# Performance work log

Measured on AMD Instinct MI355X. Metric: run time of the kernel, lower is better.

## Reference

```python
import jax, jax.numpy as jnp
import numpy as np
from jax import lax

K = 3      # reassembly kernel size
UP = 2     # upsample factor


def setup_inputs() -> dict:
    key = jax.random.key(0)
    ks = jax.random.split(key, 4)
    N, C, H, W = 4, 256, 128, 128
    outC = 256
    x = jax.random.normal(ks[0], (N, C, H, W), dtype=jnp.float32)
    w_down = jax.random.normal(ks[1], (C // 4, C), dtype=jnp.float32) * 0.05
    b_down = jnp.zeros((C // 4,), dtype=jnp.float32)
    w_enc = jax.random.normal(ks[2], (UP * UP * K * K, C // 4, K, K), dtype=jnp.float32) * 0.05
    b_enc = jnp.zeros((UP * UP * K * K,), dtype=jnp.float32)
    w_out = jax.random.normal(ks[3], (outC, C), dtype=jnp.float32) * 0.05
    b_out = jnp.zeros((outC,), dtype=jnp.float32)
    return {"x": x, "w_down": w_down, "b_down": b_down,
            "w_enc": w_enc, "b_enc": b_enc, "w_out": w_out, "b_out": b_out}


def _carafe_upsample(x, w_down, b_down, w_enc, b_enc, w_out, b_out):
    N, C, H, W = x.shape
    k2, up2 = K * K, UP * UP
    # kernel prediction branch: 1x1 down conv, 3x3 encoder conv
    t = jnp.einsum('oc,nchw->nohw', w_down, x) + b_down[None, :, None, None]
    enc = lax.conv_general_dilated(
        t, w_enc, window_strides=(1, 1), padding=((K // 2, K // 2), (K // 2, K // 2)),
        dimension_numbers=('NCHW', 'OIHW', 'NCHW')) + b_enc[None, :, None, None]
    # torch encoder channel layout is kk*up2 + ij; pixel_shuffle + softmax(dim=1)
    # + unfold(up,up) is equivalent to softmax over the k^2 axis here.
    enc = enc.reshape(N, k2, up2, H, W)
    kernel = jax.nn.softmax(enc, axis=1)                 # [N,k2,up2,H,W]
    kernel = kernel.transpose(0, 3, 4, 1, 2)             # [N,H,W,k2,up2]
    # extract kxk patches (zero pad), ordering di*K+dj matches torch unfold
    pad = K // 2
    xp = jnp.pad(x, ((0, 0), (0, 0), (pad, pad), (pad, pad)))
    patches = jnp.stack([xp[:, :, di:di + H, dj:dj + W]
                         for di in range(K) for dj in range(K)], axis=-1)  # [N,C,H,W,k2]
    # per-pixel reassembly matmul
    out = jnp.einsum('nchwk,nhwkq->nchwq', patches, kernel)  # [N,C,H,W,up2]
    # pixel_shuffle: channel index c*up2 + i*UP + j -> (h*UP+i, w*UP+j)
    out = out.reshape(N, C, H, W, UP, UP).transpose(0, 1, 2, 4, 3, 5)
    out = out.reshape(N, C, H * UP, W * UP)
    # final 1x1 conv
    return jnp.einsum('oc,nchw->nohw', w_out, out) + b_out[None, :, None, None]


def reference(x, w_down, b_down, w_enc, b_enc, w_out, b_out):
    return _carafe_upsample(x, w_down, b_down, w_enc, b_enc, w_out, b_out)
```

## Files before the change

### kernel.cpp

```cpp
#include <hip/hip_runtime.h>
#include <hip/hip_bf16.h>
#include <stddef.h>

typedef __attribute__((ext_vector_type(8))) short short8;
typedef __attribute__((ext_vector_type(4))) short short4v;
typedef __attribute__((ext_vector_type(4))) unsigned short ushort4v;
typedef __attribute__((ext_vector_type(4))) float floatx4;

#define N_ 4
#define C_ 256
#define H_ 128
#define W_ 128
#define HW_ (H_*W_)
#define NPX_ (N_*HW_)
#define E_ 36
#define OC_ 256

static __device__ __forceinline__ unsigned short f2bf(float f) {
    union { float f; unsigned u; } v; v.f = f;
    unsigned r = v.u + 0x7fff + ((v.u >> 16) & 1);
    return (unsigned short)(r >> 16);
}
static __device__ __forceinline__ float bf2f(unsigned short s) {
    union { unsigned u; float f; } v; v.u = ((unsigned)s) << 16;
    return v.f;
}

__global__ __launch_bounds__(256) void k_prep(const float* __restrict__ wo,
                                              const float* __restrict__ wd,
                                              short* __restrict__ wcomb,
                                              const float* __restrict__ we,
                                              unsigned short* __restrict__ wBT) {
    int bx = blockIdx.x;
    if (bx < 80) {
        int i = (bx * 256 + threadIdx.x) * 4;
        int row = i >> 8, c = i & 255;
        const float* src = (row < 256) ? &wo[row * 256 + c] : &wd[(row - 256) * 256 + c];
        float4 v = *(const float4*)src;
        short4v s;
        s.x = (short)f2bf(v.x); s.y = (short)f2bf(v.y);
        s.z = (short)f2bf(v.z); s.w = (short)f2bf(v.w);
        *(short4v*)&wcomb[i] = s;
    } else {
        int idx = (bx - 80) * 256 + threadIdx.x;
        if (idx < 48 * 576) {
            int e = idx / 576;
            int k = idx - e * 576;
            int tap = k >> 6, c = k & 63;
            float v = (e < E_) ? we[((size_t)e * 64 + c) * 9 + tap] : 0.f;
            wBT[idx] = f2bf(v);
        }
    }
}

__global__ __launch_bounds__(512, 3) void k_gemm(
    const float* __restrict__ x, const short* __restrict__ wcomb,
    const float* __restrict__ bd,
    unsigned short* __restrict__ Gq, unsigned short* __restrict__ t)
{
    __shared__ short Asm[2][320 * 40];
    __shared__ short Bsm[2][128 * 40];

    int tid = threadIdx.x;
    int bx = blockIdx.x;
    int n = bx >> 7;
    int px0 = (bx & 127) * 128;

    int lane = tid & 63;
    int wave = tid >> 6;
    int wm = wave >> 2, wn = wave & 3;

    int ao = tid >> 1, ah = tid & 1;
    int bpx = tid & 127, bcq = tid >> 7;
    bool hasExtra = (tid < 128);

    const float* xb = x + (size_t)n * C_ * HW_ + px0 + bpx;
    const short* wr  = wcomb + ao * C_ + ah * 16;
    const short* wr2 = wcomb + (256 + (tid >> 1)) * C_ + (tid & 1) * 16;

    short8 a0, a1, a2, a3;
    float xg[8];

    auto issue = [&](int c0) {
        a0 = *(const short8*)(wr + c0);
        a1 = *(const short8*)(wr + c0 + 8);
        if (hasExtra) {
            a2 = *(const short8*)(wr2 + c0);
            a3 = *(const short8*)(wr2 + c0 + 8);
        }
        #pragma unroll
        for (int j = 0; j < 8; j++)
            xg[j] = xb[(size_t)(c0 + bcq * 8 + j) * HW_];
    };
    auto commit = [&](int buf) {
        short* ad = &Asm[buf][ao * 40 + ah * 16];
        *(short8*)ad = a0;
        *(short8*)(ad + 8) = a1;
        if (hasExtra) {
            short* ad2 = &Asm[buf][(256 + (tid >> 1)) * 40 + (tid & 1) * 16];
            *(short8*)ad2 = a2;
            *(short8*)(ad2 + 8) = a3;
        }
        short8 bv;
        #pragma unroll
        for (int j = 0; j < 8; j++) bv[j] = (short)f2bf(xg[j]);
        *(short8*)&Bsm[buf][bpx * 40 + bcq * 8] = bv;
    };

    floatx4 acc[10][2];
    #pragma unroll
    for (int fm = 0; fm < 10; fm++) {
        acc[fm][0] = (floatx4)0.f;
        acc[fm][1] = (floatx4)0.f;
    }

    issue(0);
    commit(0);
    __syncthreads();

    for (int kc = 0; kc < 8; kc++) {
        int cur = kc & 1;
        if (kc < 7) issue((kc + 1) * 32);
        short8 bfrag[2];
        #pragma unroll
        for (int fn = 0; fn < 2; fn++) {
            int col = wn * 32 + fn * 16 + (lane & 15);
            bfrag[fn] = *(const short8*)&Bsm[cur][col * 40 + (lane >> 4) * 8];
        }
        #pragma unroll
        for (int fm = 0; fm < 10; fm++) {
            int rbase = (fm < 8) ? (wm * 128 + fm * 16) : (256 + wm * 32 + (fm - 8) * 16);
            int row = rbase + (lane & 15);
            short8 af = *(const short8*)&Asm[cur][row * 40 + (lane >> 4) * 8];
            acc[fm][0] = __builtin_amdgcn_mfma_f32_16x16x32_bf16(af, bfrag[0], acc[fm][0], 0, 0, 0);
            acc[fm][1] = __builtin_amdgcn_mfma_f32_16x16x32_bf16(af, bfrag[1], acc[fm][1], 0, 0, 0);
        }
        if (kc < 7) {
            commit(cur ^ 1);
            __syncthreads();
        }
    }
    #pragma unroll
    for (int fm = 0; fm < 8; fm++) {
        int oq = wm * 32 + fm * 4 + (lane >> 4);
        #pragma unroll
        for (int fn = 0; fn < 2; fn++) {
            int col = px0 + wn * 32 + fn * 16 + (lane & 15);
            ushort4v v;
            v.x = f2bf(acc[fm][fn][0]);
            v.y = f2bf(acc[fm][fn][1]);
            v.z = f2bf(acc[fm][fn][2]);
            v.w = f2bf(acc[fm][fn][3]);
            *(ushort4v*)&Gq[(((size_t)n * 64 + oq) * HW_ + col) * 4] = v;
        }
    }
    #pragma unroll
    for (int f8 = 0; f8 < 2; f8++) {
        int ot = wm * 32 + f8 * 16 + ((lane >> 4) << 2);
        float b0 = bd[ot + 0], b1 = bd[ot + 1], b2 = bd[ot + 2], b3 = bd[ot + 3];
        #pragma unroll
        for (int fn = 0; fn < 2; fn++) {
            int col = px0 + wn * 32 + fn * 16 + (lane & 15);
            ushort4v r;
            r.x = f2bf(acc[8 + f8][fn][0] + b0);
            r.y = f2bf(acc[8 + f8][fn][1] + b1);
            r.z = f2bf(acc[8 + f8][fn][2] + b2);
            r.w = f2bf(acc[8 + f8][fn][3] + b3);
            *(ushort4v*)&t[((size_t)n * HW_ + col) * 64 + ot] = r;
        }
    }
}

__global__ __launch_bounds__(256) void k_enc(
    const unsigned short* __restrict__ t, const unsigned short* __restrict__ wBT,
    const float* __restrict__ be, float* __restrict__ kern)
{
    __shared__ unsigned short Tl[198 * 64];
    __shared__ float El[64 * 48];

    int bx = blockIdx.x;
    int n = bx >> 8, h = (bx >> 1) & 127, wh = bx & 1;
    int w0 = wh * 64;
    int tid = threadIdx.x;

    for (int idx = tid; idx < 1584; idx += 256) {
        int r = idx >> 3, ch = idx & 7;
        int di = r / 66, rr = r - di * 66;
        int hh = h + di - 1, ww = w0 + rr - 1;
        short8 v = {0,0,0,0,0,0,0,0};
        if (hh >= 0 && hh < H_ && ww >= 0 && ww < W_)
            v = *(const short8*)&t[((size_t)(n * H_ + hh) * W_ + ww) * 64 + ch * 8];
        int us = (r * 64 + ch * 8) ^ ((r & 7) << 3);
        *(short8*)&Tl[us] = v;
    }
    __syncthreads();

    int lane = tid & 63, wave = tid >> 6;
    int m0 = wave * 16;

    floatx4 acc[3];
    acc[0] = (floatx4)0.f; acc[1] = (floatx4)0.f; acc[2] = (floatx4)0.f;

    int pxl = m0 + (lane & 15);
    int kq = (lane >> 4) * 8;
    #pragma unroll
    for (int kc = 0; kc < 18; kc++) {
        const int tap = kc >> 1, chalf = kc & 1;
        const int di = tap / 3, dj = tap % 3;
        int r = di * 66 + pxl + dj;
        int us = (r * 64 + chalf * 32 + kq) ^ ((r & 7) << 3);
        short8 af = *(const short8*)&Tl[us];
        #pragma unroll
        for (int fn = 0; fn < 3; fn++) {
            int nn = fn * 16 + (lane & 15);
            short8 bf = *(const short8*)&wBT[(size_t)nn * 576 + kc * 32 + kq];
            acc[fn] = __builtin_amdgcn_mfma_f32_16x16x32_bf16(af, bf, acc[fn], 0, 0, 0);
        }
    }
    #pragma unroll
    for (int fn = 0; fn < 3; fn++)
        #pragma unroll
        for (int i = 0; i < 4; i++) {
            int px = m0 + (lane >> 4) * 4 + i;
            El[px * 48 + fn * 16 + (lane & 15)] = acc[fn][i];
        }
    __syncthreads();

    int sp = tid >> 2, q = tid & 3;
    float l[9];
    #pragma unroll
    for (int k = 0; k < 9; k++) l[k] = El[sp * 48 + k * 4 + q] + be[k * 4 + q];
    float m = l[0];
    #pragma unroll
    for (int k = 1; k < 9; k++) m = fmaxf(m, l[k]);
    float ex[9], s = 0.f;
    #pragma unroll
    for (int k = 0; k < 9; k++) { ex[k] = __expf(l[k] - m); s += ex[k]; }
    float inv = 1.f / s;
    int pxg = n * HW_ + h * W_ + w0 + sp;
    #pragma unroll
    for (int k = 0; k < 9; k++)
        kern[(size_t)(k * 4 + q) * NPX_ + pxg] = ex[k] * inv;
}

__global__ __launch_bounds__(256) void k_up(
    const unsigned short* __restrict__ Gq, const float* __restrict__ kern,
    const float* __restrict__ bo, float* __restrict__ y)
{
    int bx = blockIdx.x;
    int x7 = bx & 7;
    int g  = bx >> 3;
    int hbhi = g & 7;
    int og = (g >> 3) & 7;
    int n  = g >> 6;
    int hb = hbhi * 8 + x7;

    int tid = threadIdx.x;
    int h = hb * 2 + (tid >> 7);
    int w = tid & 127;
    int idxp = n * HW_ + h * W_ + w;

    float kv[36];
    #pragma unroll
    for (int e = 0; e < E_; e++)
        kv[e] = kern[(size_t)e * NPX_ + idxp];

    int off[9]; bool val[9];
    #pragma unroll
    for (int di = 0; di < 3; di++) {
        int hh = h + di - 1;
        bool hvv = (hh >= 0 && hh < H_);
        int hc = hvv ? hh : h;
        #pragma unroll
        for (int dj = 0; dj < 3; dj++) {
            int ww = w + dj - 1;
            bool wvv = (ww >= 0 && ww < W_);
            int wc = wvv ? ww : w;
            off[di * 3 + dj] = hc * W_ + wc;
            val[di * 3 + dj] = hvv && wvv;
        }
    }

    const unsigned short* Gb = Gq + ((size_t)n * 64 + og * 8) * HW_ * 4;
    size_t ybase = ((size_t)n * OC_ + og * 32) * (4 * HW_) + (size_t)(2 * h) * 256 + 2 * w;

    #pragma unroll 2
    for (int j = 0; j < 8; j++) {
        const unsigned short* Gj = Gb + (size_t)j * HW_ * 4;
        float b0 = bo[og * 32 + j * 4 + 0];
        float b1 = bo[og * 32 + j * 4 + 1];
        float b2 = bo[og * 32 + j * 4 + 2];
        float b3 = bo[og * 32 + j * 4 + 3];
        float a[4][4];
        #pragma unroll
        for (int s = 0; s < 4; s++) { a[0][s] = b0; a[1][s] = b1; a[2][s] = b2; a[3][s] = b3; }
        #pragma unroll
        for (int k = 0; k < 9; k++) {
            ushort4v gv = *(const ushort4v*)(Gj + (size_t)off[k] * 4);
            float g0 = val[k] ? bf2f(gv.x) : 0.f;
            float g1 = val[k] ? bf2f(gv.y) : 0.f;
            float g2 = val[k] ? bf2f(gv.z) : 0.f;
            float g3 = val[k] ? bf2f(gv.w) : 0.f;
            #pragma unroll
            for (int s = 0; s < 4; s++) {
                float kw = kv[k * 4 + s];
                a[0][s] = fmaf(g0, kw, a[0][s]);
                a[1][s] = fmaf(g1, kw, a[1][s]);
                a[2][s] = fmaf(g2, kw, a[2][s]);
                a[3][s] = fmaf(g3, kw, a[3][s]);
            }
        }
        #pragma unroll
        for (int i = 0; i < 4; i++) {
            float* yp = y + ybase + (size_t)(j * 4 + i) * (4 * HW_);
            float2 r0; r0.x = a[i][0]; r0.y = a[i][1];
            float2 r1; r1.x = a[i][2]; r1.y = a[i][3];
            *(float2*)yp = r0;
            *(float2*)(yp + 256) = r1;
        }
    }
}

extern "C" void kernel_launch(void* const* d_in, const int* in_sizes, int n_in,
                              void* d_out, int out_size, void* d_ws, size_t ws_size,
                              hipStream_t stream) {
    const float* x  = (const float*)d_in[0];
    const float* wd = (const float*)d_in[1];
    const float* bd = (const float*)d_in[2];
    const float* we = (const float*)d_in[3];
    const float* be = (const float*)d_in[4];
    const float* wo = (const float*)d_in[5];
    const float* bo = (const float*)d_in[6];
    float* y = (float*)d_out;

    unsigned short* t = (unsigned short*)d_ws;
    float* kern = (float*)(t + (size_t)NPX_ * 64);
    short* wcomb = (short*)(kern + (size_t)E_ * NPX_);
    unsigned short* wBT = (unsigned short*)(wcomb + (size_t)320 * C_);
    unsigned short* Gq  = wBT + (size_t)48 * 576;

    k_prep<<<188,  256, 0, stream>>>(wo, wd, wcomb, we, wBT);
    k_gemm<<<512,  512, 0, stream>>>(x, wcomb, bd, Gq, t);
    k_enc <<<1024, 256, 0, stream>>>(t, wBT, be, kern);
    k_up  <<<2048, 256, 0, stream>>>(Gq, kern, bo, y);
}
```

Before: 148.8 us.

## Widen enc conv tile to full row and prefetch weights into registers

The encoder 3x3 conv kernel now processes a full 128-pixel row per block instead of half a row. Each wave computes two M fragments, which shrinks halo reloads from the 3-row neighbourhood and halves the block count. B-operand weight fragments are prefetched into a 3-slot register ring two k-steps ahead rather than loaded from global memory right before each MFMA. The LDS tile is reused for the softmax staging buffer with a padded stride of 49. The trade-off is more registers and LDS per block and fewer blocks, which may lower occupancy.

```diff
diff --git a/kernel.cpp b/kernel.cpp
--- a/kernel.cpp
+++ b/kernel.cpp
@@ -175,18 +175,26 @@
     const unsigned short* __restrict__ t, const unsigned short* __restrict__ wBT,
     const float* __restrict__ be, float* __restrict__ kern)
 {
-    __shared__ unsigned short Tl[198 * 64];
-    __shared__ float El[64 * 48];
+    __shared__ short Tl[390 * 64];
+    float* El = (float*)Tl;
 
     int bx = blockIdx.x;
-    int n = bx >> 8, h = (bx >> 1) & 127, wh = bx & 1;
-    int w0 = wh * 64;
+    int n = bx >> 7, h = bx & 127;
     int tid = threadIdx.x;
-
-    for (int idx = tid; idx < 1584; idx += 256) {
+    int lane = tid & 63, wave = tid >> 6;
+
+    short8 bpre[3][3];
+    const unsigned short* wB0 = wBT + (size_t)(lane & 15) * 576 + (lane >> 4) * 8;
+    #pragma unroll
+    for (int p = 0; p < 2; p++)
+        #pragma unroll
+        for (int fn = 0; fn < 3; fn++)
+            bpre[p][fn] = *(const short8*)(wB0 + fn * 16 * 576 + p * 32);
+
+    for (int idx = tid; idx < 3120; idx += 256) {
         int r = idx >> 3, ch = idx & 7;
-        int di = r / 66, rr = r - di * 66;
-        int hh = h + di - 1, ww = w0 + rr - 1;
+        int di = r / 130, rr = r - di * 130;
+        int hh = h + di - 1, ww = rr - 1;
         short8 v = {0,0,0,0,0,0,0,0};
         if (hh >= 0 && hh < H_ && ww >= 0 && ww < W_)
             v = *(const short8*)&t[((size_t)(n * H_ + hh) * W_ + ww) * 64 + ch * 8];
@@ -195,52 +203,69 @@
     }
     __syncthreads();
 
-    int lane = tid & 63, wave = tid >> 6;
-    int m0 = wave * 16;
-
-    floatx4 acc[3];
-    acc[0] = (floatx4)0.f; acc[1] = (floatx4)0.f; acc[2] = (floatx4)0.f;
-
-    int pxl = m0 + (lane & 15);
+    floatx4 acc[2][3];
+    #pragma unroll
+    for (int mf = 0; mf < 2; mf++)
+        #pragma unroll
+        for (int fn = 0; fn < 3; fn++)
+            acc[mf][fn] = (floatx4)0.f;
+
+    int pxw = wave * 32 + (lane & 15);
     int kq = (lane >> 4) * 8;
+
     #pragma unroll
     for (int kc = 0; kc < 18; kc++) {
+        if (kc < 16) {
+            int slot = (kc + 2) % 3;
+            #pragma unroll
+            for (int fn = 0; fn < 3; fn++)
+                bpre[slot][fn] = *(const short8*)(wB0 + fn * 16 * 576 + (kc + 2) * 32);
+        }
+        const int cur = kc % 3;
         const int tap = kc >> 1, chalf = kc & 1;
         const int di = tap / 3, dj = tap % 3;
-        int r = di * 66 + pxl + dj;
-        int us = (r * 64 + chalf * 32 + kq) ^ ((r & 7) << 3);
-        short8 af = *(const short8*)&Tl[us];
-        #pragma unroll
-        for (int fn = 0; fn < 3; fn++) {
-            int nn = fn * 16 + (lane & 15);
-            short8 bf = *(const short8*)&wBT[(size_t)nn * 576 + kc * 32 + kq];
-            acc[fn] = __builtin_amdgcn_mfma_f32_16x16x32_bf16(af, bf, acc[fn], 0, 0, 0);
-        }
-    }
-    #pragma unroll
-    for (int fn = 0; fn < 3; fn++)
-        #pragma unroll
-        for (int i = 0; i < 4; i++) {
-            int px = m0 + (lane >> 4) * 4 + i;
-            El[px * 48 + fn * 16 + (lane & 15)] = acc[fn][i];
-        }
+        #pragma unroll
+        for (int mf = 0; mf < 2; mf++) {
+            int r = di * 130 + pxw + mf * 16 + dj;
+            int us = (r * 64 + chalf * 32 + kq) ^ ((r & 7) << 3);
+            short8 af = *(const short8*)&Tl[us];
+            #pragma unroll
+            for (int fn = 0; fn < 3; fn++)
+                acc[mf][fn] = __builtin_amdgcn_mfma_f32_16x16x32_bf16(af, bpre[cur][fn], acc[mf][fn], 0, 0, 0);
+        }
+    }
     __syncthreads();
 
-    int sp = tid >> 2, q = tid & 3;
-    float l[9];
-    #pragma unroll
-    for (int k = 0; k < 9; k++) l[k] = El[sp * 48 + k * 4 + q] + be[k * 4 + q];
-    float m = l[0];
-    #pragma unroll
-    for (int k = 1; k < 9; k++) m = fmaxf(m, l[k]);
-    float ex[9], s = 0.f;
-    #pragma unroll
-    for (int k = 0; k < 9; k++) { ex[k] = __expf(l[k] - m); s += ex[k]; }
-    float inv = 1.f / s;
-    int pxg = n * HW_ + h * W_ + w0 + sp;
-    #pragma unroll
-    for (int k = 0; k < 9; k++)
-        kern[(size_t)(k * 4 + q) * NPX_ + pxg] = ex[k] * inv;
+    #pragma unroll
+    for (int mf = 0; mf < 2; mf++)
+        #pragma unroll
+        for (int fn = 0; fn < 3; fn++)
+            #pragma unroll
+            for (int i = 0; i < 4; i++) {
+                int px = wave * 32 + mf * 16 + (lane >> 4) * 4 + i;
+                El[px * 49 + fn * 16 + (lane & 15)] = acc[mf][fn][i];
+            }
+    __syncthreads();
+
+    int sp = tid >> 1;
+    int pxg = n * HW_ + h * W_ + sp;
+    #pragma unroll
+    for (int qq = 0; qq < 2; qq++) {
+        int q = (tid & 1) * 2 + qq;
+        float l[9];
+        #pragma unroll
+        for (int k = 0; k < 9; k++) l[k] = El[sp * 49 + k * 4 + q] + be[k * 4 + q];
+        float m = l[0];
+        #pragma unroll
+        for (int k = 1; k < 9; k++) m = fmaxf(m, l[k]);
+        float ex[9], s = 0.f;
+        #pragma unroll
+        for (int k = 0; k < 9; k++) { ex[k] = __expf(l[k] - m); s += ex[k]; }
+        float inv = 1.f / s;
+        #pragma unroll
+        for (int k = 0; k < 9; k++)
+            kern[(size_t)(k * 4 + q) * NPX_ + pxg] = ex[k] * inv;
+    }
 }
 
 __global__ __launch_bounds__(256) void k_up(
@@ -341,6 +366,6 @@
 
     k_prep<<<188,  256, 0, stream>>>(wo, wd, wcomb, we, wBT);
     k_gemm<<<512,  512, 0, stream>>>(x, wcomb, bd, Gq, t);
-    k_enc <<<1024, 256, 0, stream>>>(t, wBT, be, kern);
+    k_enc <<<512,  256, 0, stream>>>(t, wBT, be, kern);
     k_up  <<<2048, 256, 0, stream>>>(Gq, kern, bo, y);
 }
```

After: 138.8 us. 1.07x faster.
